# Kernel optimization log

Measured on AMD Instinct MI355X. Metric: run time of the kernel, lower is better.

The kernel has to match this reference:

```python
import jax, jax.numpy as jnp
import numpy as np

N_RAYS = 65536
N_SAMPLES = 2_097_152
HID = 64
L_PTS, L_DIR = 10, 4
STEP = 5e-3
WHITE_BKGD = True


def posenc(x, L):
    # x [..., 3] -> [..., 3 + 6L]
    freqs = (2.0 ** jnp.arange(L)).astype(x.dtype)            # [L]
    ang = x[..., None, :] * freqs[:, None]                     # [..., L, 3]
    enc = jnp.concatenate([jnp.sin(ang), jnp.cos(ang)], -1)   # [..., L, 6]
    return jnp.concatenate([x, enc.reshape(x.shape[:-1] + (6 * L,))], -1)


def setup_inputs() -> dict:
    key = jax.random.key(0)
    ks = jax.random.split(key, 12)
    rays_o = jax.random.normal(ks[0], (N_RAYS, 3), jnp.float32)
    viewdirs = jax.random.normal(ks[1], (N_RAYS, 3), jnp.float32)
    viewdirs = viewdirs / jnp.linalg.norm(viewdirs, axis=-1, keepdims=True)
    ray_indices = jnp.sort(jax.random.randint(ks[2], (N_SAMPLES,), 0, N_RAYS, jnp.int32))
    t_starts = jax.random.uniform(ks[3], (N_SAMPLES,), jnp.float32, 0.0, 4.0)
    t_ends = t_starts + STEP

    def w(k, shape):
        return jax.random.normal(k, shape, jnp.float32) / jnp.sqrt(shape[0])

    D_PTS = 3 + 6 * L_PTS   # 63
    D_DIR = 3 + 6 * L_DIR   # 27
    return dict(
        rays_o=rays_o, viewdirs=viewdirs, t_starts=t_starts, t_ends=t_ends,
        W1=w(ks[4], (D_PTS, HID)), b1=jnp.zeros((HID,), jnp.float32),
        W2=w(ks[5], (HID, HID)), b2=jnp.zeros((HID,), jnp.float32),
        Wd=w(ks[6], (HID, 1)), bd=jnp.zeros((1,), jnp.float32),
        Wf=w(ks[7], (HID, HID)), bf=jnp.zeros((HID,), jnp.float32),
        Wr1=w(ks[8], (HID + D_DIR, HID)), br1=jnp.zeros((HID,), jnp.float32),
        Wr2=w(ks[9], (HID, 3)), br2=jnp.zeros((3,), jnp.float32),
        ray_indices=ray_indices,
    )


def reference(rays_o, viewdirs, t_starts, t_ends,
              W1, b1, W2, b2, Wd, bd, Wf, bf, Wr1, br1, Wr2, br2,
              ray_indices):
    t_mid = 0.5 * (t_starts + t_ends)                     # [S]
    o = rays_o[ray_indices]                               # gather [S,3]
    d = viewdirs[ray_indices]                             # gather [S,3]
    pts = o + d * t_mid[:, None]                          # [S,3]

    # small NeRF MLP (self.net): sigma + view-dependent rgb
    h = jax.nn.relu(posenc(pts, L_PTS) @ W1 + b1)
    h = jax.nn.relu(h @ W2 + b2)
    sigma = jax.nn.relu((h @ Wd + bd)[:, 0])              # relu(density)
    feat = h @ Wf + bf
    hd = jax.nn.relu(jnp.concatenate([feat, posenc(d, L_DIR)], -1) @ Wr1 + br1)
    rgb = jax.nn.sigmoid(hd @ Wr2 + br2)                  # [S,3]

    alpha = 1.0 - jnp.exp(-sigma * (t_ends - t_starts))   # [S], in [0,1)

    # per-ray exclusive transmittance via segment exclusive cumsum in log space
    log1m = jnp.log1p(-jnp.clip(alpha, 0.0, 1.0 - 1e-7))  # <= 0
    excl = jnp.cumsum(log1m) - log1m                      # global exclusive cumsum
    counts = jax.ops.segment_sum(jnp.ones_like(ray_indices), ray_indices, N_RAYS)
    start_idx = jnp.cumsum(counts) - counts               # first sample of each ray
    offset = jnp.where(counts > 0, excl[jnp.clip(start_idx, 0, N_SAMPLES - 1)], 0.0)
    T = jnp.exp(excl - offset[ray_indices])               # transmittance [S]
    w = T * alpha                                         # render weights [S]

    colors = jax.ops.segment_sum(w[:, None] * rgb, ray_indices, N_RAYS)   # [R,3]
    opac = jax.ops.segment_sum(w, ray_indices, N_RAYS)                    # [R]
    depth = jax.ops.segment_sum(w * t_mid, ray_indices, N_RAYS)           # [R]

    bkgd = 1.0 if WHITE_BKGD else 0.0
    colors = colors + (1.0 - opac)[:, None] * bkgd
    return colors, opac[:, None], depth[:, None]
```

## Files before the change

### kernel.cpp

```cpp
#include <hip/hip_runtime.h>
#include <math.h>

#define NR 65536
#define NS 2097152

typedef __attribute__((ext_vector_type(4))) float f32x4;
typedef __attribute__((ext_vector_type(8))) short short8;

#define RSTRIDE 36
#define GSTRIDE (16 * 36 + 4)


__device__ __forceinline__ uint packbf(float a, float b) {
    __bf16 lo = (__bf16)a, hi = (__bf16)b;
    ushort ul = __builtin_bit_cast(ushort, lo);
    ushort uh = __builtin_bit_cast(ushort, hi);
    return (uint)ul | ((uint)uh << 16);
}
__device__ __forceinline__ float bflo(uint u) { return __builtin_bit_cast(float, u << 16); }

__global__ void init_bounds(int* __restrict__ start, int* __restrict__ end) {
    int r = blockIdx.x * blockDim.x + threadIdx.x;
    if (r < NR) { start[r] = 0; end[r] = 0; }
}

__global__ void find_bounds(const int* __restrict__ ridx,
                            int* __restrict__ start, int* __restrict__ end) {
    int i = blockIdx.x * blockDim.x + threadIdx.x;
    if (i >= NS) return;
    int r = ridx[i];
    if (i == 0 || ridx[i - 1] != r) start[r] = i;
    if (i == NS - 1 || ridx[i + 1] != r) end[r] = i + 1;
}

__global__ void direnc_kernel(const float* __restrict__ viewdirs,
                              uint4* __restrict__ dtab) {
    int r = blockIdx.x * blockDim.x + threadIdx.x;
    if (r >= NR) return;
    float dx = viewdirs[3 * r + 0], dy = viewdirs[3 * r + 1], dz = viewdirs[3 * r + 2];
    float de[32];
    de[0] = dx; de[1] = dy; de[2] = dz;
    float sx = __sinf(dx), cx = __cosf(dx);
    float sy = __sinf(dy), cy = __cosf(dy);
    float sz = __sinf(dz), cz = __cosf(dz);
    #pragma unroll
    for (int l = 0; l < 4; ++l) {
        de[3 + 6 * l + 0] = sx; de[3 + 6 * l + 1] = sy; de[3 + 6 * l + 2] = sz;
        de[3 + 6 * l + 3] = cx; de[3 + 6 * l + 4] = cy; de[3 + 6 * l + 5] = cz;
        float nsx = 2.0f * sx * cx, nsy = 2.0f * sy * cy, nsz = 2.0f * sz * cz;
        cx = fmaf(-2.0f * sx, sx, 1.0f);
        cy = fmaf(-2.0f * sy, sy, 1.0f);
        cz = fmaf(-2.0f * sz, sz, 1.0f);
        sx = nsx; sy = nsy; sz = nsz;
    }
    #pragma unroll
    for (int k = 27; k < 32; ++k) de[k] = 0.0f;
    #pragma unroll
    for (int c = 0; c < 4; ++c) {
        uint4 q = make_uint4(packbf(de[8 * c + 0], de[8 * c + 1]),
                             packbf(de[8 * c + 2], de[8 * c + 3]),
                             packbf(de[8 * c + 4], de[8 * c + 5]),
                             packbf(de[8 * c + 6], de[8 * c + 7]));
        dtab[(size_t)r * 4 + c] = q;
    }
}

__global__ void build_frags(const float* __restrict__ W1, const float* __restrict__ W2,
                            const float* __restrict__ Wf, const float* __restrict__ Wr1,
                            const float* __restrict__ Wd, const float* __restrict__ Wr2,
                            uint4* __restrict__ wfrag) {
    int t = blockIdx.x * blockDim.x + threadIdx.x;
    if (t >= 40 * 64) return;
    int f = t >> 6, lane = t & 63;
    int c = lane & 15;
    uint q[4];
    if (f < 36) {
        const float* W; int kmax, fl;
        if (f < 8)       { W = W1;  kmax = 63; fl = f; }
        else if (f < 16) { W = W2;  kmax = 64; fl = f - 8; }
        else if (f < 24) { W = Wf;  kmax = 64; fl = f - 16; }
        else             { W = Wr1; kmax = 91; fl = f - 24; }
        int ks = fl >> 2, ft = fl & 3;
        int n = ft * 16 + c;
        int kb = ks * 32 + ((lane >> 4) * 8);
        #pragma unroll
        for (int j = 0; j < 4; ++j) {
            int k0 = kb + 2 * j, k1 = k0 + 1;
            float v0 = (k0 < kmax) ? W[k0 * 64 + n] : 0.0f;
            float v1 = (k1 < kmax) ? W[k1 * 64 + n] : 0.0f;
            q[j] = packbf(v0, v1);
        }
    } else if (f < 38) {
        int kb = (f - 36) * 32 + ((lane >> 4) * 8);
        #pragma unroll
        for (int j = 0; j < 4; ++j) {
            float v0 = (c == 0) ? Wd[kb + 2 * j] : 0.0f;
            float v1 = (c == 0) ? Wd[kb + 2 * j + 1] : 0.0f;
            q[j] = packbf(v0, v1);
        }
    } else {
        int kb = (f - 38) * 32 + ((lane >> 4) * 8);
        #pragma unroll
        for (int j = 0; j < 4; ++j) {
            float v0 = (c < 3) ? Wr2[(kb + 2 * j) * 3 + c] : 0.0f;
            float v1 = (c < 3) ? Wr2[(kb + 2 * j + 1) * 3 + c] : 0.0f;
            q[j] = packbf(v0, v1);
        }
    }
    wfrag[(size_t)f * 64 + lane] = make_uint4(q[0], q[1], q[2], q[3]);
}


template <int KS, bool RELU, bool SIGMA, bool DIRB>
__device__ __forceinline__ void dense_layer(uint* S, const uint4* __restrict__ wfrag,
                                            int fb, const float* __restrict__ bias,
                                            float bd0, uint rbase, uint wbA, uint wbB,
                                            int lane, const uint4 (&dirB)[4]) {
    const int g = lane >> 4;
    uint4 wf[KS * 4];
    #pragma unroll
    for (int i = 0; i < KS * 4; ++i) wf[i] = wfrag[(size_t)(fb + i) * 64 + lane];
    uint4 wsg[2];
    if constexpr (SIGMA) {
        wsg[0] = wfrag[36 * 64 + lane];
        wsg[1] = wfrag[37 * 64 + lane];
    }
    float4 bfr[4];
    #pragma unroll
    for (int ft = 0; ft < 4; ++ft)
        bfr[ft] = *(const float4*)(bias + 16 * ft + 4 * g);

    #pragma unroll
    for (int st = 0; st < 4; ++st) {
        const uint stoff = (uint)st * (uint)GSTRIDE;
        uint4 B[KS];
        #pragma unroll
        for (int ks = 0; ks < KS; ++ks) {
            if (DIRB && ks == KS - 1) B[ks] = dirB[st];
            else B[ks] = *(const uint4*)&S[rbase + stoff + 16u * (uint)ks];
        }
        f32x4 acc[4];
        #pragma unroll
        for (int ft = 0; ft < 4; ++ft)
            acc[ft] = (f32x4){bfr[ft].x, bfr[ft].y, bfr[ft].z, bfr[ft].w};
        f32x4 sacc;
        if constexpr (SIGMA) sacc = (f32x4){(g == 0) ? bd0 : 0.0f, 0.0f, 0.0f, 0.0f};
        #pragma unroll
        for (int ks = 0; ks < KS; ++ks) {
            short8 bv = __builtin_bit_cast(short8, B[ks]);
            #pragma unroll
            for (int ft = 0; ft < 4; ++ft)
                acc[ft] = __builtin_amdgcn_mfma_f32_16x16x32_bf16(
                    __builtin_bit_cast(short8, wf[ks * 4 + ft]), bv, acc[ft], 0, 0, 0);
            if constexpr (SIGMA)
                sacc = __builtin_amdgcn_mfma_f32_16x16x32_bf16(
                    __builtin_bit_cast(short8, wsg[ks]), bv, sacc, 0, 0, 0);
        }
        #pragma unroll
        for (int ft = 0; ft < 4; ++ft) {
            float a0 = acc[ft][0], a1 = acc[ft][1], a2 = acc[ft][2], a3 = acc[ft][3];
            if constexpr (RELU) {
                a0 = fmaxf(a0, 0.0f); a1 = fmaxf(a1, 0.0f);
                a2 = fmaxf(a2, 0.0f); a3 = fmaxf(a3, 0.0f);
            }
            uint2 v = make_uint2(packbf(a0, a1), packbf(a2, a3));
            uint base = (ft & 1) ? wbB : wbA;
            *(uint2*)&S[base + stoff + 16u * (uint)(ft >> 1)] = v;
        }
        if constexpr (SIGMA) {
            if (g == 0) S[rbase + stoff + 33u] = __builtin_bit_cast(uint, sacc[0]);
        }
    }
}

__global__ __launch_bounds__(256, 4) void fused_mlp(
    const float* __restrict__ rays_o, const float* __restrict__ viewdirs,
    const float* __restrict__ t_starts, const float* __restrict__ t_ends,
    const float* __restrict__ b1, const float* __restrict__ b2,
    const float* __restrict__ bd, const float* __restrict__ bf_,
    const float* __restrict__ br1, const float* __restrict__ br2,
    const int* __restrict__ ridx, const uint4* __restrict__ wfrag,
    const uint4* __restrict__ dtab, uint2* __restrict__ rgba)
{
    __shared__ uint S[16 * GSTRIDE];

    const int tid = threadIdx.x;
    const int w = tid >> 6, lane = tid & 63;
    const int g = lane >> 4, s = lane & 15;
    const uint wgb = (uint)(w * 4) * (uint)GSTRIDE;
    const uint rowcol = wgb + (uint)s * (uint)RSTRIDE;
    const int sb0 = blockIdx.x * 256 + w * 64;

    int ridx4[4];
    #pragma unroll
    for (int st = 0; st < 4; ++st) ridx4[st] = ridx[sb0 + st * 16 + s];
    uint4 dirB[4];
    #pragma unroll
    for (int st = 0; st < 4; ++st) dirB[st] = dtab[(size_t)ridx4[st] * 4 + g];

    const int si = sb0 + g * 16 + s;
    const int rr = ridx4[g];
    float ts = t_starts[si], te = t_ends[si];
    float tm = 0.5f * (ts + te), dtv = te - ts;
    float dx = viewdirs[3 * rr + 0], dy = viewdirs[3 * rr + 1], dz = viewdirs[3 * rr + 2];
    float px = rays_o[3 * rr + 0] + dx * tm;
    float py = rays_o[3 * rr + 1] + dy * tm;
    float pz = rays_o[3 * rr + 2] + dz * tm;

    const uint ownrow = wgb + (uint)g * (uint)GSTRIDE + (uint)s * (uint)RSTRIDE;
    const uint rbase = rowcol + 4u * (uint)g;
    const uint wbA = rowcol + 2u * (uint)g;
    const uint wbB = wbA + 8u;

    {
        float enc[64];
        enc[0] = px; enc[1] = py; enc[2] = pz;
        float sx = __sinf(px), cx = __cosf(px);
        float sy = __sinf(py), cy = __cosf(py);
        float sz = __sinf(pz), cz = __cosf(pz);
        #pragma unroll
        for (int l = 0; l < 10; ++l) {
            enc[3 + 6 * l + 0] = sx; enc[3 + 6 * l + 1] = sy; enc[3 + 6 * l + 2] = sz;
            enc[3 + 6 * l + 3] = cx; enc[3 + 6 * l + 4] = cy; enc[3 + 6 * l + 5] = cz;
            float nsx = 2.0f * sx * cx, nsy = 2.0f * sy * cy, nsz = 2.0f * sz * cz;
            cx = fmaf(-2.0f * sx, sx, 1.0f);
            cy = fmaf(-2.0f * sy, sy, 1.0f);
            cz = fmaf(-2.0f * sz, sz, 1.0f);
            sx = nsx; sy = nsy; sz = nsz;
        }
        enc[63] = 0.0f;
        #pragma unroll
        for (int ch = 0; ch < 8; ++ch) {
            uint4 q = make_uint4(packbf(enc[8 * ch + 0], enc[8 * ch + 1]),
                                 packbf(enc[8 * ch + 2], enc[8 * ch + 3]),
                                 packbf(enc[8 * ch + 4], enc[8 * ch + 5]),
                                 packbf(enc[8 * ch + 6], enc[8 * ch + 7]));
            *(uint4*)&S[ownrow + 4u * (uint)ch] = q;
        }
    }
    S[ownrow + 32] = __builtin_bit_cast(uint, dtv);

    float bd0 = bd[0];
    uint4 dummy[4];

    dense_layer<2, true,  false, false>(S, wfrag,  0, b1,  0.0f, rbase, wbA, wbB, lane, dummy);
    dense_layer<2, true,  false, false>(S, wfrag,  8, b2,  0.0f, rbase, wbA, wbB, lane, dummy);
    dense_layer<2, false, true,  false>(S, wfrag, 16, bf_, bd0,  rbase, wbA, wbB, lane, dummy);
    dense_layer<3, true,  false, true >(S, wfrag, 24, br1, 0.0f, rbase, wbA, wbB, lane, dirB);

    {
        uint4 wr0 = wfrag[38 * 64 + lane], wr1f = wfrag[39 * 64 + lane];
        float c0 = br2[0], c1 = br2[1], c2 = br2[2];
        #pragma unroll
        for (int st = 0; st < 4; ++st) {
            const uint stoff = (uint)st * (uint)GSTRIDE;
            uint4 B0 = *(const uint4*)&S[rbase + stoff];
            uint4 B1 = *(const uint4*)&S[rbase + stoff + 16u];
            f32x4 acc = (g == 0) ? (f32x4){c0, c1, c2, 0.0f}
                                 : (f32x4){0.0f, 0.0f, 0.0f, 0.0f};
            acc = __builtin_amdgcn_mfma_f32_16x16x32_bf16(
                __builtin_bit_cast(short8, wr0), __builtin_bit_cast(short8, B0), acc, 0, 0, 0);
            acc = __builtin_amdgcn_mfma_f32_16x16x32_bf16(
                __builtin_bit_cast(short8, wr1f), __builtin_bit_cast(short8, B1), acc, 0, 0, 0);
            if (lane < 16) {
                float sg = fmaxf(__builtin_bit_cast(float, S[rbase + stoff + 33u]), 0.0f);
                float dte = __builtin_bit_cast(float, S[rbase + stoff + 32u]);
                float alpha = 1.0f - __expf(-sg * dte);
                float r0 = 1.0f / (1.0f + __expf(-acc[0]));
                float r1 = 1.0f / (1.0f + __expf(-acc[1]));
                float r2 = 1.0f / (1.0f + __expf(-acc[2]));
                uint2 o;
                o.x = packbf(r0, r1);
                o.y = packbf(r2, alpha);
                rgba[sb0 + st * 16 + lane] = o;
            }
        }
    }
}

__global__ void render_kernel(const uint2* __restrict__ rgba,
                              const float* __restrict__ t_starts,
                              const float* __restrict__ t_ends,
                              const int* __restrict__ start,
                              const int* __restrict__ end,
                              float* __restrict__ out)
{
    int r = blockIdx.x * blockDim.x + threadIdx.x;
    if (r >= NR) return;
    int sb = start[r], e = end[r];
    float T = 1.0f, c0 = 0.0f, c1 = 0.0f, c2 = 0.0f, op = 0.0f, dp = 0.0f;
    for (int i = sb; i < e; ++i) {
        uint2 q = rgba[i];
        float vr = bflo(q.x & 0xffffu), vg = bflo(q.x >> 16);
        float vb = bflo(q.y & 0xffffu), va = bflo(q.y >> 16);
        float wgt = T * va;
        float tmid = 0.5f * (t_starts[i] + t_ends[i]);
        c0 += wgt * vr; c1 += wgt * vg; c2 += wgt * vb;
        op += wgt; dp += wgt * tmid;
        T *= (1.0f - va);
    }
    float bg = 1.0f - op;
    c0 += bg; c1 += bg; c2 += bg;
    out[3 * r + 0] = c0;
    out[3 * r + 1] = c1;
    out[3 * r + 2] = c2;
    out[3 * NR + r] = op;
    out[4 * NR + r] = dp;
}

extern "C" void kernel_launch(void* const* d_in, const int* in_sizes, int n_in,
                              void* d_out, int out_size, void* d_ws, size_t ws_size,
                              hipStream_t stream) {
    const float* rays_o   = (const float*)d_in[0];
    const float* viewdirs = (const float*)d_in[1];
    const float* t_starts = (const float*)d_in[2];
    const float* t_ends   = (const float*)d_in[3];
    const float* W1  = (const float*)d_in[4];
    const float* b1  = (const float*)d_in[5];
    const float* W2  = (const float*)d_in[6];
    const float* b2  = (const float*)d_in[7];
    const float* Wd  = (const float*)d_in[8];
    const float* bd  = (const float*)d_in[9];
    const float* Wf  = (const float*)d_in[10];
    const float* bf_ = (const float*)d_in[11];
    const float* Wr1 = (const float*)d_in[12];
    const float* br1 = (const float*)d_in[13];
    const float* Wr2 = (const float*)d_in[14];
    const float* br2 = (const float*)d_in[15];
    const int* ridx  = (const int*)d_in[16];
    float* out = (float*)d_out;

    char* ws = (char*)d_ws;
    uint2* rgba = (uint2*)ws;
    int* start = (int*)(ws + (size_t)NS * 8);
    int* end   = start + NR;
    uint4* wfrag = (uint4*)(ws + (size_t)NS * 8 + (size_t)NR * 8);
    uint4* dtab  = (uint4*)(ws + (size_t)NS * 8 + (size_t)NR * 8 + 40 * 64 * 16);

    build_frags<<<10, 256, 0, stream>>>(W1, W2, Wf, Wr1, Wd, Wr2, wfrag);
    direnc_kernel<<<NR / 256, 256, 0, stream>>>(viewdirs, dtab);
    init_bounds<<<NR / 256, 256, 0, stream>>>(start, end);
    find_bounds<<<NS / 256, 256, 0, stream>>>(ridx, start, end);
    fused_mlp<<<NS / 256, 256, 0, stream>>>(
        rays_o, viewdirs, t_starts, t_ends,
        b1, b2, bd, bf_, br1, br2, ridx, wfrag, dtab, rgba);
    render_kernel<<<NR / 256, 256, 0, stream>>>(rgba, t_starts, t_ends, start, end, out);
}
```

Before: 159.6 us.

## Merge setup kernels, cache t_mid for render, add MFMA priority and packed math

Folds build_frags, direnc_kernel and init_bounds into a single setup_kernel launch, which removes two kernel launches. The MLP kernel now writes t_mid to a workspace array, so render reads one float per sample instead of two. The MFMA loop is wrapped in s_setprio hints, the positional-encoding recurrence uses 2-wide float vectors, and the dt/sigma reads are merged into a single uint2 LDS load. The trade-off is an extra global store of 4 bytes per sample in the MLP kernel.

```diff
diff --git a/kernel.cpp b/kernel.cpp
--- a/kernel.cpp
+++ b/kernel.cpp
@@ -5,6 +5,7 @@
 #define NS 2097152
 
 typedef __attribute__((ext_vector_type(4))) float f32x4;
+typedef __attribute__((ext_vector_type(2))) float f32x2;
 typedef __attribute__((ext_vector_type(8))) short short8;
 
 #define RSTRIDE 36
@@ -18,11 +19,6 @@
     return (uint)ul | ((uint)uh << 16);
 }
 __device__ __forceinline__ float bflo(uint u) { return __builtin_bit_cast(float, u << 16); }
-
-__global__ void init_bounds(int* __restrict__ start, int* __restrict__ end) {
-    int r = blockIdx.x * blockDim.x + threadIdx.x;
-    if (r < NR) { start[r] = 0; end[r] = 0; }
-}
 
 __global__ void find_bounds(const int* __restrict__ ridx,
                             int* __restrict__ start, int* __restrict__ end) {
@@ -33,81 +29,86 @@
     if (i == NS - 1 || ridx[i + 1] != r) end[r] = i + 1;
 }
 
-__global__ void direnc_kernel(const float* __restrict__ viewdirs,
-                              uint4* __restrict__ dtab) {
-    int r = blockIdx.x * blockDim.x + threadIdx.x;
-    if (r >= NR) return;
-    float dx = viewdirs[3 * r + 0], dy = viewdirs[3 * r + 1], dz = viewdirs[3 * r + 2];
-    float de[32];
-    de[0] = dx; de[1] = dy; de[2] = dz;
-    float sx = __sinf(dx), cx = __cosf(dx);
-    float sy = __sinf(dy), cy = __cosf(dy);
-    float sz = __sinf(dz), cz = __cosf(dz);
-    #pragma unroll
-    for (int l = 0; l < 4; ++l) {
-        de[3 + 6 * l + 0] = sx; de[3 + 6 * l + 1] = sy; de[3 + 6 * l + 2] = sz;
-        de[3 + 6 * l + 3] = cx; de[3 + 6 * l + 4] = cy; de[3 + 6 * l + 5] = cz;
-        float nsx = 2.0f * sx * cx, nsy = 2.0f * sy * cy, nsz = 2.0f * sz * cz;
-        cx = fmaf(-2.0f * sx, sx, 1.0f);
-        cy = fmaf(-2.0f * sy, sy, 1.0f);
-        cz = fmaf(-2.0f * sz, sz, 1.0f);
-        sx = nsx; sy = nsy; sz = nsz;
-    }
-    #pragma unroll
-    for (int k = 27; k < 32; ++k) de[k] = 0.0f;
-    #pragma unroll
-    for (int c = 0; c < 4; ++c) {
-        uint4 q = make_uint4(packbf(de[8 * c + 0], de[8 * c + 1]),
-                             packbf(de[8 * c + 2], de[8 * c + 3]),
-                             packbf(de[8 * c + 4], de[8 * c + 5]),
-                             packbf(de[8 * c + 6], de[8 * c + 7]));
-        dtab[(size_t)r * 4 + c] = q;
-    }
-}
-
-__global__ void build_frags(const float* __restrict__ W1, const float* __restrict__ W2,
-                            const float* __restrict__ Wf, const float* __restrict__ Wr1,
-                            const float* __restrict__ Wd, const float* __restrict__ Wr2,
-                            uint4* __restrict__ wfrag) {
-    int t = blockIdx.x * blockDim.x + threadIdx.x;
-    if (t >= 40 * 64) return;
-    int f = t >> 6, lane = t & 63;
-    int c = lane & 15;
-    uint q[4];
-    if (f < 36) {
-        const float* W; int kmax, fl;
-        if (f < 8)       { W = W1;  kmax = 63; fl = f; }
-        else if (f < 16) { W = W2;  kmax = 64; fl = f - 8; }
-        else if (f < 24) { W = Wf;  kmax = 64; fl = f - 16; }
-        else             { W = Wr1; kmax = 91; fl = f - 24; }
-        int ks = fl >> 2, ft = fl & 3;
-        int n = ft * 16 + c;
-        int kb = ks * 32 + ((lane >> 4) * 8);
-        #pragma unroll
-        for (int j = 0; j < 4; ++j) {
-            int k0 = kb + 2 * j, k1 = k0 + 1;
-            float v0 = (k0 < kmax) ? W[k0 * 64 + n] : 0.0f;
-            float v1 = (k1 < kmax) ? W[k1 * 64 + n] : 0.0f;
-            q[j] = packbf(v0, v1);
-        }
-    } else if (f < 38) {
-        int kb = (f - 36) * 32 + ((lane >> 4) * 8);
-        #pragma unroll
-        for (int j = 0; j < 4; ++j) {
-            float v0 = (c == 0) ? Wd[kb + 2 * j] : 0.0f;
-            float v1 = (c == 0) ? Wd[kb + 2 * j + 1] : 0.0f;
-            q[j] = packbf(v0, v1);
-        }
+__global__ void setup_kernel(const float* __restrict__ viewdirs,
+                             uint4* __restrict__ dtab,
+                             int* __restrict__ start, int* __restrict__ end,
+                             const float* __restrict__ W1, const float* __restrict__ W2,
+                             const float* __restrict__ Wf, const float* __restrict__ Wr1,
+                             const float* __restrict__ Wd, const float* __restrict__ Wr2,
+                             uint4* __restrict__ wfrag) {
+    int b = blockIdx.x, tid = threadIdx.x;
+    if (b < 256) {
+        int r = b * 256 + tid;
+        float dx = viewdirs[3 * r + 0], dy = viewdirs[3 * r + 1], dz = viewdirs[3 * r + 2];
+        float de[32];
+        de[0] = dx; de[1] = dy; de[2] = dz;
+        float sx = __sinf(dx), cx = __cosf(dx);
+        float sy = __sinf(dy), cy = __cosf(dy);
+        float sz = __sinf(dz), cz = __cosf(dz);
+        #pragma unroll
+        for (int l = 0; l < 4; ++l) {
+            de[3 + 6 * l + 0] = sx; de[3 + 6 * l + 1] = sy; de[3 + 6 * l + 2] = sz;
+            de[3 + 6 * l + 3] = cx; de[3 + 6 * l + 4] = cy; de[3 + 6 * l + 5] = cz;
+            float nsx = 2.0f * sx * cx, nsy = 2.0f * sy * cy, nsz = 2.0f * sz * cz;
+            cx = fmaf(-2.0f * sx, sx, 1.0f);
+            cy = fmaf(-2.0f * sy, sy, 1.0f);
+            cz = fmaf(-2.0f * sz, sz, 1.0f);
+            sx = nsx; sy = nsy; sz = nsz;
+        }
+        #pragma unroll
+        for (int k = 27; k < 32; ++k) de[k] = 0.0f;
+        #pragma unroll
+        for (int c = 0; c < 4; ++c) {
+            uint4 q = make_uint4(packbf(de[8 * c + 0], de[8 * c + 1]),
+                                 packbf(de[8 * c + 2], de[8 * c + 3]),
+                                 packbf(de[8 * c + 4], de[8 * c + 5]),
+                                 packbf(de[8 * c + 6], de[8 * c + 7]));
+            dtab[(size_t)r * 4 + c] = q;
+        }
+    } else if (b < 512) {
+        int r = (b - 256) * 256 + tid;
+        start[r] = 0; end[r] = 0;
     } else {
-        int kb = (f - 38) * 32 + ((lane >> 4) * 8);
-        #pragma unroll
-        for (int j = 0; j < 4; ++j) {
-            float v0 = (c < 3) ? Wr2[(kb + 2 * j) * 3 + c] : 0.0f;
-            float v1 = (c < 3) ? Wr2[(kb + 2 * j + 1) * 3 + c] : 0.0f;
-            q[j] = packbf(v0, v1);
-        }
-    }
-    wfrag[(size_t)f * 64 + lane] = make_uint4(q[0], q[1], q[2], q[3]);
+        int t = (b - 512) * 256 + tid;
+        if (t >= 40 * 64) return;
+        int f = t >> 6, lane = t & 63;
+        int c = lane & 15;
+        uint q[4];
+        if (f < 36) {
+            const float* W; int kmax, fl;
+            if (f < 8)       { W = W1;  kmax = 63; fl = f; }
+            else if (f < 16) { W = W2;  kmax = 64; fl = f - 8; }
+            else if (f < 24) { W = Wf;  kmax = 64; fl = f - 16; }
+            else             { W = Wr1; kmax = 91; fl = f - 24; }
+            int ks = fl >> 2, ft = fl & 3;
+            int n = ft * 16 + c;
+            int kb = ks * 32 + ((lane >> 4) * 8);
+            #pragma unroll
+            for (int j = 0; j < 4; ++j) {
+                int k0 = kb + 2 * j, k1 = k0 + 1;
+                float v0 = (k0 < kmax) ? W[k0 * 64 + n] : 0.0f;
+                float v1 = (k1 < kmax) ? W[k1 * 64 + n] : 0.0f;
+                q[j] = packbf(v0, v1);
+            }
+        } else if (f < 38) {
+            int kb = (f - 36) * 32 + ((lane >> 4) * 8);
+            #pragma unroll
+            for (int j = 0; j < 4; ++j) {
+                float v0 = (c == 0) ? Wd[kb + 2 * j] : 0.0f;
+                float v1 = (c == 0) ? Wd[kb + 2 * j + 1] : 0.0f;
+                q[j] = packbf(v0, v1);
+            }
+        } else {
+            int kb = (f - 38) * 32 + ((lane >> 4) * 8);
+            #pragma unroll
+            for (int j = 0; j < 4; ++j) {
+                float v0 = (c < 3) ? Wr2[(kb + 2 * j) * 3 + c] : 0.0f;
+                float v1 = (c < 3) ? Wr2[(kb + 2 * j + 1) * 3 + c] : 0.0f;
+                q[j] = packbf(v0, v1);
+            }
+        }
+        wfrag[(size_t)f * 64 + lane] = make_uint4(q[0], q[1], q[2], q[3]);
+    }
 }
 
 
@@ -145,6 +146,7 @@
             acc[ft] = (f32x4){bfr[ft].x, bfr[ft].y, bfr[ft].z, bfr[ft].w};
         f32x4 sacc;
         if constexpr (SIGMA) sacc = (f32x4){(g == 0) ? bd0 : 0.0f, 0.0f, 0.0f, 0.0f};
+        __builtin_amdgcn_s_setprio(1);
         #pragma unroll
         for (int ks = 0; ks < KS; ++ks) {
             short8 bv = __builtin_bit_cast(short8, B[ks]);
@@ -156,6 +158,7 @@
                 sacc = __builtin_amdgcn_mfma_f32_16x16x32_bf16(
                     __builtin_bit_cast(short8, wsg[ks]), bv, sacc, 0, 0, 0);
         }
+        __builtin_amdgcn_s_setprio(0);
         #pragma unroll
         for (int ft = 0; ft < 4; ++ft) {
             float a0 = acc[ft][0], a1 = acc[ft][1], a2 = acc[ft][2], a3 = acc[ft][3];
@@ -180,7 +183,8 @@
     const float* __restrict__ bd, const float* __restrict__ bf_,
     const float* __restrict__ br1, const float* __restrict__ br2,
     const int* __restrict__ ridx, const uint4* __restrict__ wfrag,
-    const uint4* __restrict__ dtab, uint2* __restrict__ rgba)
+    const uint4* __restrict__ dtab, uint2* __restrict__ rgba,
+    float* __restrict__ tmarr)
 {
     __shared__ uint S[16 * GSTRIDE];
 
@@ -206,6 +210,7 @@
     float px = rays_o[3 * rr + 0] + dx * tm;
     float py = rays_o[3 * rr + 1] + dy * tm;
     float pz = rays_o[3 * rr + 2] + dz * tm;
+    tmarr[si] = tm;
 
     const uint ownrow = wgb + (uint)g * (uint)GSTRIDE + (uint)s * (uint)RSTRIDE;
     const uint rbase = rowcol + 4u * (uint)g;
@@ -215,18 +220,18 @@
     {
         float enc[64];
         enc[0] = px; enc[1] = py; enc[2] = pz;
-        float sx = __sinf(px), cx = __cosf(px);
-        float sy = __sinf(py), cy = __cosf(py);
+        f32x2 sxy = {__sinf(px), __sinf(py)};
+        f32x2 cxy = {__cosf(px), __cosf(py)};
         float sz = __sinf(pz), cz = __cosf(pz);
         #pragma unroll
         for (int l = 0; l < 10; ++l) {
-            enc[3 + 6 * l + 0] = sx; enc[3 + 6 * l + 1] = sy; enc[3 + 6 * l + 2] = sz;
-            enc[3 + 6 * l + 3] = cx; enc[3 + 6 * l + 4] = cy; enc[3 + 6 * l + 5] = cz;
-            float nsx = 2.0f * sx * cx, nsy = 2.0f * sy * cy, nsz = 2.0f * sz * cz;
-            cx = fmaf(-2.0f * sx, sx, 1.0f);
-            cy = fmaf(-2.0f * sy, sy, 1.0f);
+            enc[3 + 6 * l + 0] = sxy.x; enc[3 + 6 * l + 1] = sxy.y; enc[3 + 6 * l + 2] = sz;
+            enc[3 + 6 * l + 3] = cxy.x; enc[3 + 6 * l + 4] = cxy.y; enc[3 + 6 * l + 5] = cz;
+            f32x2 nsxy = 2.0f * sxy * cxy;
+            cxy = 1.0f - 2.0f * sxy * sxy;
+            float nsz = 2.0f * sz * cz;
             cz = fmaf(-2.0f * sz, sz, 1.0f);
-            sx = nsx; sy = nsy; sz = nsz;
+            sxy = nsxy; sz = nsz;
         }
         enc[63] = 0.0f;
         #pragma unroll
@@ -263,8 +268,9 @@
             acc = __builtin_amdgcn_mfma_f32_16x16x32_bf16(
                 __builtin_bit_cast(short8, wr1f), __builtin_bit_cast(short8, B1), acc, 0, 0, 0);
             if (lane < 16) {
-                float sg = fmaxf(__builtin_bit_cast(float, S[rbase + stoff + 33u]), 0.0f);
-                float dte = __builtin_bit_cast(float, S[rbase + stoff + 32u]);
+                uint2 meta = *(const uint2*)&S[rbase + stoff + 32u];
+                float dte = __builtin_bit_cast(float, meta.x);
+                float sg = fmaxf(__builtin_bit_cast(float, meta.y), 0.0f);
                 float alpha = 1.0f - __expf(-sg * dte);
                 float r0 = 1.0f / (1.0f + __expf(-acc[0]));
                 float r1 = 1.0f / (1.0f + __expf(-acc[1]));
@@ -279,8 +285,7 @@
 }
 
 __global__ void render_kernel(const uint2* __restrict__ rgba,
-                              const float* __restrict__ t_starts,
-                              const float* __restrict__ t_ends,
+                              const float* __restrict__ tmarr,
                               const int* __restrict__ start,
                               const int* __restrict__ end,
                               float* __restrict__ out)
@@ -291,10 +296,10 @@
     float T = 1.0f, c0 = 0.0f, c1 = 0.0f, c2 = 0.0f, op = 0.0f, dp = 0.0f;
     for (int i = sb; i < e; ++i) {
         uint2 q = rgba[i];
+        float tmid = tmarr[i];
         float vr = bflo(q.x & 0xffffu), vg = bflo(q.x >> 16);
         float vb = bflo(q.y & 0xffffu), va = bflo(q.y >> 16);
         float wgt = T * va;
-        float tmid = 0.5f * (t_starts[i] + t_ends[i]);
         c0 += wgt * vr; c1 += wgt * vg; c2 += wgt * vb;
         op += wgt; dp += wgt * tmid;
         T *= (1.0f - va);
@@ -331,18 +336,18 @@
     float* out = (float*)d_out;
 
     char* ws = (char*)d_ws;
-    uint2* rgba = (uint2*)ws;
-    int* start = (int*)(ws + (size_t)NS * 8);
-    int* end   = start + NR;
-    uint4* wfrag = (uint4*)(ws + (size_t)NS * 8 + (size_t)NR * 8);
-    uint4* dtab  = (uint4*)(ws + (size_t)NS * 8 + (size_t)NR * 8 + 40 * 64 * 16);
-
-    build_frags<<<10, 256, 0, stream>>>(W1, W2, Wf, Wr1, Wd, Wr2, wfrag);
-    direnc_kernel<<<NR / 256, 256, 0, stream>>>(viewdirs, dtab);
-    init_bounds<<<NR / 256, 256, 0, stream>>>(start, end);
+    uint2* rgba  = (uint2*)ws;
+    float* tmarr = (float*)(ws + (size_t)NS * 8);
+    int* start   = (int*)(ws + (size_t)NS * 12);
+    int* end     = start + NR;
+    uint4* wfrag = (uint4*)(ws + (size_t)NS * 12 + (size_t)NR * 8);
+    uint4* dtab  = (uint4*)(ws + (size_t)NS * 12 + (size_t)NR * 8 + 40 * 64 * 16);
+
+    setup_kernel<<<522, 256, 0, stream>>>(viewdirs, dtab, start, end,
+                                          W1, W2, Wf, Wr1, Wd, Wr2, wfrag);
     find_bounds<<<NS / 256, 256, 0, stream>>>(ridx, start, end);
     fused_mlp<<<NS / 256, 256, 0, stream>>>(
         rays_o, viewdirs, t_starts, t_ends,
-        b1, b2, bd, bf_, br1, br2, ridx, wfrag, dtab, rgba);
-    render_kernel<<<NR / 256, 256, 0, stream>>>(rgba, t_starts, t_ends, start, end, out);
-}
+        b1, b2, bd, bf_, br1, br2, ridx, wfrag, dtab, rgba, tmarr);
+    render_kernel<<<NR / 256, 256, 0, stream>>>(rgba, tmarr, start, end, out);
+}
```

After: 144.6 us. 1.1x faster.
